# Kernel optimization log

Hardware: AMD Instinct MI355X
Metric: run time of the kernel (lower is better)

Reference implementation:

```python
import jax, jax.numpy as jnp
import numpy as np
from jax import lax

TOP_K = 4
N_GROUP = 4
TOPK_GROUP = 2
ROUTED_SCALING = 2.5
NORM_TOPK = True


def relu2(v):
    r = jax.nn.relu(v)
    return r * r


def setup_inputs() -> dict:
    key = jax.random.key(0)
    ks = jax.random.split(key, 7)
    B, S, H, E, I, IS = 2, 2048, 1024, 16, 512, 2048
    x = jax.random.normal(ks[0], (B, S, H), dtype=jnp.float32)
    router_w = jax.random.normal(ks[1], (E, H), dtype=jnp.float32) * 0.02
    bias = jnp.zeros((E,), dtype=jnp.float32)
    w_up = jax.random.normal(ks[2], (E, I, H), dtype=jnp.float32) * 0.02
    w_down = jax.random.normal(ks[3], (E, H, I), dtype=jnp.float32) * 0.02
    ws_up = jax.random.normal(ks[4], (IS, H), dtype=jnp.float32) * 0.02
    ws_down = jax.random.normal(ks[5], (H, IS), dtype=jnp.float32) * 0.02
    return {"x": x, "router_w": router_w, "bias": bias, "w_up": w_up,
            "w_down": w_down, "ws_up": ws_up, "ws_down": ws_down,
            "attn_metadata": 0}


def _route(xf, router_w, bias):
    # xf: [T, H] float32
    T = xf.shape[0]
    E = router_w.shape[0]
    logits = xf @ router_w.T                      # [T, E]
    scores = jax.nn.sigmoid(logits)
    sfc = scores + bias[None, :]                  # scores_for_choice
    # group scores: sum of top-2 within each group
    g = sfc.reshape(T, N_GROUP, E // N_GROUP)
    group_scores = lax.top_k(g, 2)[0].sum(-1)     # [T, G]
    _, gidx = lax.top_k(group_scores, TOPK_GROUP)
    gmask = jax.nn.one_hot(gidx, N_GROUP, dtype=sfc.dtype).sum(1)  # [T, G]
    smask = jnp.repeat(gmask, E // N_GROUP, axis=1)                # [T, E]
    masked = jnp.where(smask > 0, sfc, 0.0)
    _, tidx = lax.top_k(masked, TOP_K)            # [T, K]
    tw = jnp.take_along_axis(scores, tidx, axis=1)
    if NORM_TOPK:
        tw = tw / (tw.sum(-1, keepdims=True) + 1e-20)
    tw = tw * ROUTED_SCALING
    return tidx, tw


def reference(x, router_w, bias, w_up, w_down, ws_up, ws_down, attn_metadata):
    B, S, H = x.shape
    E = w_up.shape[0]
    xf = x.reshape(-1, H).astype(jnp.float32)     # [T, H]
    tidx, tw = _route(xf, router_w, bias)
    # combine weights per (token, expert): scatter-add topk weights
    T = xf.shape[0]
    comb = jnp.zeros((T, E), dtype=tw.dtype).at[jnp.arange(T)[:, None], tidx].add(tw)
    # routed experts (dense grouped form; zero combine weight == not routed)
    up = jnp.einsum('th,eih->tei', xf, w_up)      # [T, E, I]
    h = relu2(up) * comb[:, :, None]
    routed = jnp.einsum('tei,ehi->th', h, w_down) # [T, H]
    routed = routed.reshape(B, S, H).astype(x.dtype)
    # shared expert on residual
    shared = relu2(jnp.einsum('bsh,ih->bsi', x, ws_up))
    shared = jnp.einsum('bsi,hi->bsh', shared, ws_down)
    return routed + shared
```

## Files before the change

kernel.cpp:

```cpp
#include <hip/hip_runtime.h>
#include <stdint.h>

#define T_TOK 4096
#define H_DIM 1024
#define E_NUM 16
#define I_DIM 512
#define IS_DIM 2048
#define TOPK 4
#define NGRP 4
#define GSZ 4
#define MAXMT 32
#define NCHUNK 64

#define W0 524288
#define W1 1048576
#define W2 3145728
#define W3 5242880

typedef unsigned short u16;
typedef __attribute__((ext_vector_type(8))) short short8;
typedef __attribute__((ext_vector_type(4))) float f32x4;

__device__ __forceinline__ void gload16(const void* g, void* l) {
  __builtin_amdgcn_global_load_lds(
      (const __attribute__((address_space(1))) void*)g,
      (__attribute__((address_space(3))) void*)l, 16, 0, 0);
}

__device__ __forceinline__ u16 f2bf(float f) {
  union { float f; uint32_t u; } v; v.f = f;
  uint32_t u = v.u;
  uint32_t r = (u + 0x7fffu + ((u >> 16) & 1u)) >> 16;
  return (u16)r;
}

__device__ __forceinline__ float bf2f(u16 h) {
  union { uint32_t u; float f; } v; v.u = ((uint32_t)h) << 16;
  return v.f;
}

__global__ __launch_bounds__(256) void cvt_w_kernel(
    const float* __restrict__ wsu, const float* __restrict__ wsd,
    const float* __restrict__ wu, const float* __restrict__ wd,
    u16* __restrict__ wsub, u16* __restrict__ wsdb,
    u16* __restrict__ wub, u16* __restrict__ wdb) {
  int i = blockIdx.x * 256 + threadIdx.x;
  const float4* src; ushort4* dst; int base;
  if (i < W0)      { src = (const float4*)wsu; dst = (ushort4*)wsub; base = 0;  }
  else if (i < W1) { src = (const float4*)wsd; dst = (ushort4*)wsdb; base = W0; }
  else if (i < W2) { src = (const float4*)wu;  dst = (ushort4*)wub;  base = W1; }
  else             { src = (const float4*)wd;  dst = (ushort4*)wdb;  base = W2; }
  float4 v = src[i - base];
  ushort4 o;
  o.x = f2bf(v.x); o.y = f2bf(v.y); o.z = f2bf(v.z); o.w = f2bf(v.w);
  dst[i - base] = o;
}

__global__ __launch_bounds__(256) void route_kernel(
    const float* __restrict__ x, const float* __restrict__ rw,
    const float* __restrict__ bias, int* __restrict__ tidx_out,
    float* __restrict__ tw_out, u16* __restrict__ x_bf) {
  const int wave = threadIdx.x >> 6;
  const int lane = threadIdx.x & 63;
  const int t = blockIdx.x * 4 + wave;

  const float4* xr = reinterpret_cast<const float4*>(x + (size_t)t * H_DIM);
  const float4* rw4 = reinterpret_cast<const float4*>(rw);
  ushort4* xbw = reinterpret_cast<ushort4*>(x_bf + (size_t)t * H_DIM);
  float4 xv[4];
#pragma unroll
  for (int j = 0; j < 4; ++j) xv[j] = xr[lane + j * 64];
#pragma unroll
  for (int j = 0; j < 4; ++j) {
    ushort4 o;
    o.x = f2bf(xv[j].x); o.y = f2bf(xv[j].y);
    o.z = f2bf(xv[j].z); o.w = f2bf(xv[j].w);
    xbw[lane + j * 64] = o;
  }

  double acc[E_NUM];
#pragma unroll
  for (int e = 0; e < E_NUM; ++e) {
    double a = 0.0;
#pragma unroll
    for (int j = 0; j < 4; ++j) {
      float4 w = rw4[e * 256 + lane + j * 64];
      a += (double)xv[j].x * (double)w.x;
      a += (double)xv[j].y * (double)w.y;
      a += (double)xv[j].z * (double)w.z;
      a += (double)xv[j].w * (double)w.w;
    }
    acc[e] = a;
  }
#pragma unroll
  for (int e = 0; e < E_NUM; ++e) {
#pragma unroll
    for (int off = 32; off; off >>= 1) acc[e] += __shfl_xor(acc[e], off);
  }
  if (lane == 0) {
    float scores[E_NUM], sfc[E_NUM];
#pragma unroll
    for (int e = 0; e < E_NUM; ++e) {
      scores[e] = 1.0f / (1.0f + expf((float)(-acc[e])));
      sfc[e] = scores[e] + bias[e];
    }
    float gs[NGRP];
#pragma unroll
    for (int g = 0; g < NGRP; ++g) {
      float m1 = -1e30f, m2 = -1e30f;
#pragma unroll
      for (int j = 0; j < GSZ; ++j) {
        float v = sfc[g * GSZ + j];
        if (v > m1) { m2 = m1; m1 = v; } else if (v > m2) { m2 = v; }
      }
      gs[g] = m1 + m2;
    }
    int g1 = 0;
    for (int g = 1; g < NGRP; ++g) if (gs[g] > gs[g1]) g1 = g;
    int g2 = -1;
    for (int g = 0; g < NGRP; ++g) {
      if (g == g1) continue;
      if (g2 < 0 || gs[g] > gs[g2]) g2 = g;
    }
    float masked[E_NUM];
#pragma unroll
    for (int e = 0; e < E_NUM; ++e) {
      int g = e / GSZ;
      masked[e] = (g == g1 || g == g2) ? sfc[e] : 0.0f;
    }
    int tidx[TOPK]; float tw[TOPK];
#pragma unroll
    for (int k = 0; k < TOPK; ++k) {
      int best = 0; float bv = masked[0];
      for (int e = 1; e < E_NUM; ++e)
        if (masked[e] > bv) { bv = masked[e]; best = e; }
      tidx[k] = best; tw[k] = scores[best]; masked[best] = -1e30f;
    }
    float s = tw[0] + tw[1] + tw[2] + tw[3] + 1e-20f;
#pragma unroll
    for (int k = 0; k < TOPK; ++k) {
      tidx_out[t * TOPK + k] = tidx[k];
      tw_out[t * TOPK + k] = tw[k] / s * 2.5f;
    }
  }
}

__global__ __launch_bounds__(256) void hist_kernel(const int* __restrict__ tidx,
                                                   int* __restrict__ partial) {
  const int c = blockIdx.x;
  const int tid = threadIdx.x;
  const int lane = tid & 63;
  const int w = tid >> 6;
  __shared__ int h[4][E_NUM];
  const int e = tidx[c * 256 + tid];
#pragma unroll
  for (int ee = 0; ee < E_NUM; ++ee) {
    unsigned long long b = __ballot(e == ee);
    if (lane == 0) h[w][ee] = __popcll(b);
  }
  __syncthreads();
  if (tid < E_NUM)
    partial[c * E_NUM + tid] = h[0][tid] + h[1][tid] + h[2][tid] + h[3][tid];
}

__global__ __launch_bounds__(256) void prefix2_kernel(
    const int* __restrict__ partial, int* __restrict__ chunk_base,
    int* __restrict__ counts, int* __restrict__ offsets) {
  __shared__ int tot[E_NUM];
  __shared__ int offs[E_NUM];
  const int tid = threadIdx.x;
  if (tid < E_NUM) {
    int run = 0;
    for (int c = 0; c < NCHUNK; ++c) {
      chunk_base[c * E_NUM + tid] = run;
      run += partial[c * E_NUM + tid];
    }
    tot[tid] = run;
    counts[tid] = run;
  }
  __syncthreads();
  if (tid == 0) {
    int s = 0;
    for (int e = 0; e < E_NUM; ++e) { offs[e] = s; offsets[e] = s; s += tot[e]; }
    offsets[E_NUM] = s;
  }
  __syncthreads();
  for (int i = tid; i < NCHUNK * E_NUM; i += 256)
    chunk_base[i] += offs[i & 15];
}

__global__ __launch_bounds__(256) void scatter2_kernel(
    const int* __restrict__ tidx, const float* __restrict__ tw,
    const int* __restrict__ chunk_base,
    int* __restrict__ tok_g, float* __restrict__ w_g, int* __restrict__ pos_map) {
  const int c = blockIdx.x;
  const int tid = threadIdx.x;
  const int lane = tid & 63;
  const int w = tid >> 6;
  __shared__ int h[4][E_NUM];
  const int i = c * 256 + tid;
  const int e = tidx[i];
  int pre = 0;
#pragma unroll
  for (int ee = 0; ee < E_NUM; ++ee) {
    unsigned long long b = __ballot(e == ee);
    if (lane == 0) h[w][ee] = __popcll(b);
    if (ee == e) pre = __popcll(b & ((1ull << lane) - 1ull));
  }
  __syncthreads();
  int rank = pre;
  for (int ww = 0; ww < w; ++ww) rank += h[ww][e];
  const int pos = chunk_base[c * E_NUM + e] + rank;
  tok_g[pos] = i >> 2;
  w_g[pos] = tw[i];
  pos_map[i] = pos;
}

#define NB_UP 5120
__global__ __launch_bounds__(256, 3) void gemm_up(
    const u16* __restrict__ x_bf, const u16* __restrict__ wsup_bf,
    const u16* __restrict__ wup_bf, u16* __restrict__ hs, u16* __restrict__ hp,
    const int* __restrict__ counts, const int* __restrict__ offsets,
    const int* __restrict__ tok_g, const float* __restrict__ w_g) {
  __shared__ __align__(16) u16 As[2][128 * 64];
  __shared__ __align__(16) u16 Bs[2][64 * 64];

  const int cpx = gridDim.x >> 3;
  const int wg = (blockIdx.x & 7) * cpx + (blockIdx.x >> 3);
  const int q = wg / 5;
  const int r5 = wg - q * 5;
  const bool shared = (r5 == 0);

  int mt, nt, cnt, obase = 0;
  const u16* B;
  if (shared) {
    mt = q >> 5;
    nt = q & 31;
    cnt = T_TOK;
    B = wsup_bf;
  } else {
    int rid = q * 4 + (r5 - 1);
    int e = rid >> 8;
    int r = rid & 255;
    mt = r >> 3;
    nt = r & 7;
    cnt = counts[e];
    if (mt * 128 >= cnt) return;
    obase = offsets[e];
    B = wup_bf + (size_t)e * (I_DIM * H_DIM);
  }
  const int K = H_DIM;

  const int tid = threadIdx.x;
  const int srow = tid >> 3;
  const int slot = tid & 7;
  const u16* gA[4];
#pragma unroll
  for (int p = 0; p < 4; ++p) {
    int rloc = p * 32 + srow;
    int ks = ((slot ^ (rloc & 7)) << 3);
    int am = mt * 128 + rloc;
    int row;
    if (shared) row = am;
    else row = tok_g[obase + ((am < cnt) ? am : 0)];
    gA[p] = x_bf + (size_t)row * H_DIM + ks;
  }
  const u16* gB[2];
#pragma unroll
  for (int p = 0; p < 2; ++p) {
    int rloc = p * 32 + srow;
    int ks = ((slot ^ (rloc & 7)) << 3);
    gB[p] = B + (size_t)(nt * 64 + rloc) * K + ks;
  }

  const int wave = tid >> 6;
  const int lane = tid & 63;
  const int wr = wave >> 1;
  const int wc = wave & 1;
  const int frow = lane & 15;
  const int l4 = lane >> 4;

  int a_off[4][2], b_off[2][2];
#pragma unroll
  for (int m = 0; m < 4; ++m) {
    int row = wr * 64 + m * 16 + frow;
#pragma unroll
    for (int kk = 0; kk < 2; ++kk)
      a_off[m][kk] = (row << 6) + ((((kk << 2) + l4) ^ (row & 7)) << 3);
  }
#pragma unroll
  for (int n = 0; n < 2; ++n) {
    int row = wc * 32 + n * 16 + frow;
#pragma unroll
    for (int kk = 0; kk < 2; ++kk)
      b_off[n][kk] = (row << 6) + ((((kk << 2) + l4) ^ (row & 7)) << 3);
  }

  f32x4 acc[4][2];
#pragma unroll
  for (int m = 0; m < 4; ++m)
#pragma unroll
    for (int n = 0; n < 2; ++n) acc[m][n] = (f32x4)0.0f;

  const int dst = tid << 3;
  auto stage = [&](int k0, int c) {
#pragma unroll
    for (int p = 0; p < 4; ++p)
      gload16(gA[p] + k0, &As[c][(p << 11) + dst]);
#pragma unroll
    for (int p = 0; p < 2; ++p)
      gload16(gB[p] + k0, &Bs[c][(p << 11) + dst]);
  };

  const int KT = K >> 6;
  stage(0, 0);
  int cur = 0;
  for (int kt = 0; kt < KT; ++kt) {
    __syncthreads();
    if (kt + 1 < KT) stage((kt + 1) << 6, cur ^ 1);
#pragma unroll
    for (int kk = 0; kk < 2; ++kk) {
      short8 a[4], b[2];
#pragma unroll
      for (int m = 0; m < 4; ++m)
        a[m] = *reinterpret_cast<const short8*>(&As[cur][a_off[m][kk]]);
#pragma unroll
      for (int n = 0; n < 2; ++n)
        b[n] = *reinterpret_cast<const short8*>(&Bs[cur][b_off[n][kk]]);
      __builtin_amdgcn_s_setprio(1);
#pragma unroll
      for (int m = 0; m < 4; ++m)
#pragma unroll
        for (int n = 0; n < 2; ++n)
          acc[m][n] = __builtin_amdgcn_mfma_f32_16x16x32_bf16(a[m], b[n], acc[m][n], 0, 0, 0);
      __builtin_amdgcn_s_setprio(0);
    }
    cur ^= 1;
  }

  const int rbase = l4 << 2;
  const int cbase = frow;
#pragma unroll
  for (int m = 0; m < 4; ++m) {
#pragma unroll
    for (int r = 0; r < 4; ++r) {
      int lr = wr * 64 + (m << 4) + rbase + r;
      int grow = mt * 128 + lr;
      if (!shared && grow >= cnt) continue;
      float wv = shared ? 1.0f : w_g[obase + grow];
#pragma unroll
      for (int n = 0; n < 2; ++n) {
        int gc = nt * 64 + wc * 32 + (n << 4) + cbase;
        float v = acc[m][n][r];
        float tpos = fmaxf(v, 0.0f);
        float o = tpos * tpos * wv;
        if (shared) hs[(size_t)grow * IS_DIM + gc] = f2bf(o);
        else hp[(size_t)(obase + grow) * I_DIM + gc] = f2bf(o);
      }
    }
  }
}

template <int EPI>
__global__ __launch_bounds__(256, 3) void gemm_bt(
    const u16* __restrict__ Abase, const u16* __restrict__ Bbase,
    float* __restrict__ Cf, u16* __restrict__ Cb,
    int M, int N, int K,
    const int* __restrict__ counts, const int* __restrict__ offsets,
    const int* __restrict__ tok_g, const float* __restrict__ w_g,
    const int* __restrict__ pos_map, const u16* __restrict__ Rd) {
  __shared__ __align__(16) u16 As[2][128 * 64];
  __shared__ __align__(16) u16 Bs[2][64 * 64];

  const int cpx = gridDim.x >> 3;
  const int wg = (blockIdx.x & 7) * cpx + (blockIdx.x >> 3);

  const int NT = N >> 6;
  int mt, nt, cnt = M, obase = 0;
  const u16* A = Abase;
  const u16* B = Bbase;

  if constexpr (EPI == 1) {
    mt = wg / NT;
    nt = wg - mt * NT;
  } else {
    const int per_e = MAXMT * NT;
    int e = wg / per_e;
    int r = wg - e * per_e;
    mt = r / NT;
    nt = r - mt * NT;
    cnt = counts[e];
    if (mt * 128 >= cnt) return;
    obase = offsets[e];
    A = Abase + (size_t)obase * I_DIM;
    B = Bbase + (size_t)e * (H_DIM * I_DIM);
  }

  const int tid = threadIdx.x;
  const int srow = tid >> 3;
  const int slot = tid & 7;
  const u16* gA[4];
#pragma unroll
  for (int p = 0; p < 4; ++p) {
    int rloc = p * 32 + srow;
    int ks = ((slot ^ (rloc & 7)) << 3);
    int am = mt * 128 + rloc;
    if constexpr (EPI == 3) {
      gA[p] = A + (size_t)((am < cnt) ? am : 0) * K + ks;
    } else {
      gA[p] = A + (size_t)am * K + ks;
    }
  }
  const u16* gB[2];
#pragma unroll
  for (int p = 0; p < 2; ++p) {
    int rloc = p * 32 + srow;
    int ks = ((slot ^ (rloc & 7)) << 3);
    gB[p] = B + (size_t)(nt * 64 + rloc) * K + ks;
  }

  const int wave = tid >> 6;
  const int lane = tid & 63;
  const int wr = wave >> 1;
  const int wc = wave & 1;
  const int frow = lane & 15;
  const int l4 = lane >> 4;

  int a_off[4][2], b_off[2][2];
#pragma unroll
  for (int m = 0; m < 4; ++m) {
    int row = wr * 64 + m * 16 + frow;
#pragma unroll
    for (int kk = 0; kk < 2; ++kk)
      a_off[m][kk] = (row << 6) + ((((kk << 2) + l4) ^ (row & 7)) << 3);
  }
#pragma unroll
  for (int n = 0; n < 2; ++n) {
    int row = wc * 32 + n * 16 + frow;
#pragma unroll
    for (int kk = 0; kk < 2; ++kk)
      b_off[n][kk] = (row << 6) + ((((kk << 2) + l4) ^ (row & 7)) << 3);
  }

  f32x4 acc[4][2];
#pragma unroll
  for (int m = 0; m < 4; ++m)
#pragma unroll
    for (int n = 0; n < 2; ++n) acc[m][n] = (f32x4)0.0f;

  const int dst = tid << 3;
  auto stage = [&](int k0, int c) {
#pragma unroll
    for (int p = 0; p < 4; ++p)
      gload16(gA[p] + k0, &As[c][(p << 11) + dst]);
#pragma unroll
    for (int p = 0; p < 2; ++p)
      gload16(gB[p] + k0, &Bs[c][(p << 11) + dst]);
  };

  const int KT = K >> 6;
  stage(0, 0);
  int cur = 0;
  for (int kt = 0; kt < KT; ++kt) {
    __syncthreads();
    if (kt + 1 < KT) stage((kt + 1) << 6, cur ^ 1);
#pragma unroll
    for (int kk = 0; kk < 2; ++kk) {
      short8 a[4], b[2];
#pragma unroll
      for (int m = 0; m < 4; ++m)
        a[m] = *reinterpret_cast<const short8*>(&As[cur][a_off[m][kk]]);
#pragma unroll
      for (int n = 0; n < 2; ++n)
        b[n] = *reinterpret_cast<const short8*>(&Bs[cur][b_off[n][kk]]);
      __builtin_amdgcn_s_setprio(1);
#pragma unroll
      for (int m = 0; m < 4; ++m)
#pragma unroll
        for (int n = 0; n < 2; ++n)
          acc[m][n] = __builtin_amdgcn_mfma_f32_16x16x32_bf16(a[m], b[n], acc[m][n], 0, 0, 0);
      __builtin_amdgcn_s_setprio(0);
    }
    cur ^= 1;
  }

  const int rbase = l4 << 2;
  const int cbase = frow;
#pragma unroll
  for (int m = 0; m < 4; ++m) {
#pragma unroll
    for (int r = 0; r < 4; ++r) {
      int lr = wr * 64 + (m << 4) + rbase + r;
      int grow = mt * 128 + lr;
      if (EPI == 3 && grow >= cnt) continue;
      const int* pm = nullptr;
      if constexpr (EPI == 1) pm = pos_map + grow * TOPK;
#pragma unroll
      for (int n = 0; n < 2; ++n) {
        int gc = nt * 64 + wc * 32 + (n << 4) + cbase;
        float v = acc[m][n][r];
        if constexpr (EPI == 1) {
          v += bf2f(Rd[(size_t)pm[0] * H_DIM + gc]);
          v += bf2f(Rd[(size_t)pm[1] * H_DIM + gc]);
          v += bf2f(Rd[(size_t)pm[2] * H_DIM + gc]);
          v += bf2f(Rd[(size_t)pm[3] * H_DIM + gc]);
          Cf[(size_t)grow * N + gc] = v;
        } else {
          Cb[(size_t)(obase + grow) * N + gc] = f2bf(v);
        }
      }
    }
  }
}

extern "C" void kernel_launch(void* const* d_in, const int* in_sizes, int n_in,
                              void* d_out, int out_size, void* d_ws, size_t ws_size,
                              hipStream_t stream) {
  const float* x = (const float*)d_in[0];
  const float* rw = (const float*)d_in[1];
  const float* bias = (const float*)d_in[2];
  const float* w_up = (const float*)d_in[3];
  const float* w_down = (const float*)d_in[4];
  const float* ws_up = (const float*)d_in[5];
  const float* ws_down = (const float*)d_in[6];
  float* out = (float*)d_out;

  uint8_t* wsb = (uint8_t*)d_ws;
  size_t off = 0;
  auto alloc = [&](size_t bytes) {
    void* p = wsb + off;
    off += (bytes + 255) & ~(size_t)255;
    return p;
  };
  u16* x_bf = (u16*)alloc((size_t)T_TOK * H_DIM * 2);
  u16* wsup_bf = (u16*)alloc((size_t)IS_DIM * H_DIM * 2);
  u16* wsdn_bf = (u16*)alloc((size_t)H_DIM * IS_DIM * 2);
  u16* wup_bf = (u16*)alloc((size_t)E_NUM * I_DIM * H_DIM * 2);
  u16* wdn_bf = (u16*)alloc((size_t)E_NUM * H_DIM * I_DIM * 2);
  u16* hs = (u16*)alloc((size_t)T_TOK * IS_DIM * 2);
  u16* hp = (u16*)alloc((size_t)(T_TOK * TOPK + 128) * I_DIM * 2);
  u16* hp_down = (u16*)alloc((size_t)(T_TOK * TOPK + 128) * H_DIM * 2);
  int* counts = (int*)alloc(64);
  int* offsets = (int*)alloc(128);
  int* tok_g = (int*)alloc((size_t)(T_TOK * TOPK) * 4);
  float* w_g = (float*)alloc((size_t)(T_TOK * TOPK) * 4);
  int* pos_map = (int*)alloc((size_t)(T_TOK * TOPK) * 4);
  int* tidx_buf = (int*)alloc((size_t)T_TOK * TOPK * 4);
  float* tw_buf = (float*)alloc((size_t)T_TOK * TOPK * 4);
  int* partial = (int*)alloc((size_t)NCHUNK * E_NUM * 4);
  int* chunk_base = (int*)alloc((size_t)NCHUNK * E_NUM * 4);

  route_kernel<<<T_TOK / 4, 256, 0, stream>>>(x, rw, bias, tidx_buf, tw_buf, x_bf);
  hist_kernel<<<NCHUNK, 256, 0, stream>>>(tidx_buf, partial);
  prefix2_kernel<<<1, 256, 0, stream>>>(partial, chunk_base, counts, offsets);
  scatter2_kernel<<<NCHUNK, 256, 0, stream>>>(tidx_buf, tw_buf, chunk_base,
                                              tok_g, w_g, pos_map);
  cvt_w_kernel<<<W3 / 256, 256, 0, stream>>>(
      ws_up, ws_down, w_up, w_down, wsup_bf, wsdn_bf, wup_bf, wdn_bf);

  gemm_up<<<NB_UP, 256, 0, stream>>>(
      x_bf, wsup_bf, wup_bf, hs, hp, counts, offsets, tok_g, w_g);
  gemm_bt<3><<<E_NUM * MAXMT * (H_DIM / 64), 256, 0, stream>>>(
      hp, wdn_bf, nullptr, hp_down, T_TOK, H_DIM, I_DIM,
      counts, offsets, tok_g, w_g, nullptr, nullptr);
  gemm_bt<1><<<(T_TOK / 128) * (H_DIM / 64), 256, 0, stream>>>(
      hs, wsdn_bf, out, nullptr, T_TOK, H_DIM, IS_DIM,
      nullptr, nullptr, nullptr, nullptr, pos_map, hp_down);
}
```

Baseline: 194.2 us.

## Switch GEMM mainloops to 3-stage BK=32 pipeline with fine-grained vmcnt waits

Both the up-projection and generic GEMM kernels move from a double-buffered BK=64 tile to a triple-buffered BK=32 tile with a matching swizzle. Loads are issued two stages ahead, and each step waits with an explicit s_waitcnt vmcnt instead of a full __syncthreads drain. Shared memory per block drops from 48KB to 36KB, and launch bounds rise to 4 blocks per CU for better latency hiding. The trade-off is twice as many barriers and loop iterations, each with fewer MFMAs, and reliance on a hand-counted vmcnt being correct.

```diff
diff --git a/kernel.cpp b/kernel.cpp
--- a/kernel.cpp
+++ b/kernel.cpp
@@ -217,13 +217,13 @@
 }
 
 #define NB_UP 5120
-__global__ __launch_bounds__(256, 3) void gemm_up(
+__global__ __launch_bounds__(256, 4) void gemm_up(
     const u16* __restrict__ x_bf, const u16* __restrict__ wsup_bf,
     const u16* __restrict__ wup_bf, u16* __restrict__ hs, u16* __restrict__ hp,
     const int* __restrict__ counts, const int* __restrict__ offsets,
     const int* __restrict__ tok_g, const float* __restrict__ w_g) {
-  __shared__ __align__(16) u16 As[2][128 * 64];
-  __shared__ __align__(16) u16 Bs[2][64 * 64];
+  __shared__ __align__(16) u16 As[3][128 * 32];
+  __shared__ __align__(16) u16 Bs[3][64 * 32];
 
   const int cpx = gridDim.x >> 3;
   const int wg = (blockIdx.x & 7) * cpx + (blockIdx.x >> 3);
@@ -252,25 +252,23 @@
   const int K = H_DIM;
 
   const int tid = threadIdx.x;
-  const int srow = tid >> 3;
-  const int slot = tid & 7;
-  const u16* gA[4];
-#pragma unroll
-  for (int p = 0; p < 4; ++p) {
-    int rloc = p * 32 + srow;
-    int ks = ((slot ^ (rloc & 7)) << 3);
+  const int srow = tid >> 2;
+  const int sphys = tid & 3;
+  const u16* gA[2];
+#pragma unroll
+  for (int p = 0; p < 2; ++p) {
+    int rloc = p * 64 + srow;
+    int ks = ((sphys ^ ((rloc >> 1) & 3)) << 3);
     int am = mt * 128 + rloc;
     int row;
     if (shared) row = am;
     else row = tok_g[obase + ((am < cnt) ? am : 0)];
     gA[p] = x_bf + (size_t)row * H_DIM + ks;
   }
-  const u16* gB[2];
-#pragma unroll
-  for (int p = 0; p < 2; ++p) {
-    int rloc = p * 32 + srow;
-    int ks = ((slot ^ (rloc & 7)) << 3);
-    gB[p] = B + (size_t)(nt * 64 + rloc) * K + ks;
+  const u16* gB;
+  {
+    int ks = ((sphys ^ ((srow >> 1) & 3)) << 3);
+    gB = B + (size_t)(nt * 64 + srow) * K + ks;
   }
 
   const int wave = tid >> 6;
@@ -280,20 +278,16 @@
   const int frow = lane & 15;
   const int l4 = lane >> 4;
 
-  int a_off[4][2], b_off[2][2];
+  int a_off[4], b_off[2];
 #pragma unroll
   for (int m = 0; m < 4; ++m) {
     int row = wr * 64 + m * 16 + frow;
-#pragma unroll
-    for (int kk = 0; kk < 2; ++kk)
-      a_off[m][kk] = (row << 6) + ((((kk << 2) + l4) ^ (row & 7)) << 3);
+    a_off[m] = (row << 5) + ((l4 ^ ((row >> 1) & 3)) << 3);
   }
 #pragma unroll
   for (int n = 0; n < 2; ++n) {
     int row = wc * 32 + n * 16 + frow;
-#pragma unroll
-    for (int kk = 0; kk < 2; ++kk)
-      b_off[n][kk] = (row << 6) + ((((kk << 2) + l4) ^ (row & 7)) << 3);
+    b_off[n] = (row << 5) + ((l4 ^ ((row >> 1) & 3)) << 3);
   }
 
   f32x4 acc[4][2];
@@ -305,37 +299,40 @@
   const int dst = tid << 3;
   auto stage = [&](int k0, int c) {
 #pragma unroll
-    for (int p = 0; p < 4; ++p)
+    for (int p = 0; p < 2; ++p)
       gload16(gA[p] + k0, &As[c][(p << 11) + dst]);
-#pragma unroll
-    for (int p = 0; p < 2; ++p)
-      gload16(gB[p] + k0, &Bs[c][(p << 11) + dst]);
+    gload16(gB + k0, &Bs[c][dst]);
   };
 
-  const int KT = K >> 6;
+  const int KT = K >> 5;
   stage(0, 0);
-  int cur = 0;
+  stage(32, 1);
+  int cb = 0, sb = 2;
   for (int kt = 0; kt < KT; ++kt) {
-    __syncthreads();
-    if (kt + 1 < KT) stage((kt + 1) << 6, cur ^ 1);
-#pragma unroll
-    for (int kk = 0; kk < 2; ++kk) {
-      short8 a[4], b[2];
-#pragma unroll
-      for (int m = 0; m < 4; ++m)
-        a[m] = *reinterpret_cast<const short8*>(&As[cur][a_off[m][kk]]);
+    if (kt < KT - 1) {
+      asm volatile("s_waitcnt vmcnt(3)" ::: "memory");
+    } else {
+      asm volatile("s_waitcnt vmcnt(0)" ::: "memory");
+    }
+    __builtin_amdgcn_s_barrier();
+    __builtin_amdgcn_sched_barrier(0);
+    if (kt + 2 < KT) stage((kt + 2) << 5, sb);
+    short8 a[4], b[2];
+#pragma unroll
+    for (int m = 0; m < 4; ++m)
+      a[m] = *reinterpret_cast<const short8*>(&As[cb][a_off[m]]);
+#pragma unroll
+    for (int n = 0; n < 2; ++n)
+      b[n] = *reinterpret_cast<const short8*>(&Bs[cb][b_off[n]]);
+    __builtin_amdgcn_s_setprio(1);
+#pragma unroll
+    for (int m = 0; m < 4; ++m)
 #pragma unroll
       for (int n = 0; n < 2; ++n)
-        b[n] = *reinterpret_cast<const short8*>(&Bs[cur][b_off[n][kk]]);
-      __builtin_amdgcn_s_setprio(1);
-#pragma unroll
-      for (int m = 0; m < 4; ++m)
-#pragma unroll
-        for (int n = 0; n < 2; ++n)
-          acc[m][n] = __builtin_amdgcn_mfma_f32_16x16x32_bf16(a[m], b[n], acc[m][n], 0, 0, 0);
-      __builtin_amdgcn_s_setprio(0);
-    }
-    cur ^= 1;
+        acc[m][n] = __builtin_amdgcn_mfma_f32_16x16x32_bf16(a[m], b[n], acc[m][n], 0, 0, 0);
+    __builtin_amdgcn_s_setprio(0);
+    cb = (cb == 2) ? 0 : cb + 1;
+    sb = (sb == 2) ? 0 : sb + 1;
   }
 
   const int rbase = l4 << 2;
@@ -362,15 +359,15 @@
 }
 
 template <int EPI>
-__global__ __launch_bounds__(256, 3) void gemm_bt(
+__global__ __launch_bounds__(256, 4) void gemm_bt(
     const u16* __restrict__ Abase, const u16* __restrict__ Bbase,
     float* __restrict__ Cf, u16* __restrict__ Cb,
     int M, int N, int K,
     const int* __restrict__ counts, const int* __restrict__ offsets,
     const int* __restrict__ tok_g, const float* __restrict__ w_g,
     const int* __restrict__ pos_map, const u16* __restrict__ Rd) {
-  __shared__ __align__(16) u16 As[2][128 * 64];
-  __shared__ __align__(16) u16 Bs[2][64 * 64];
+  __shared__ __align__(16) u16 As[3][128 * 32];
+  __shared__ __align__(16) u16 Bs[3][64 * 32];
 
   const int cpx = gridDim.x >> 3;
   const int wg = (blockIdx.x & 7) * cpx + (blockIdx.x >> 3);
@@ -397,13 +394,13 @@
   }
 
   const int tid = threadIdx.x;
-  const int srow = tid >> 3;
-  const int slot = tid & 7;
-  const u16* gA[4];
-#pragma unroll
-  for (int p = 0; p < 4; ++p) {
-    int rloc = p * 32 + srow;
-    int ks = ((slot ^ (rloc & 7)) << 3);
+  const int srow = tid >> 2;
+  const int sphys = tid & 3;
+  const u16* gA[2];
+#pragma unroll
+  for (int p = 0; p < 2; ++p) {
+    int rloc = p * 64 + srow;
+    int ks = ((sphys ^ ((rloc >> 1) & 3)) << 3);
     int am = mt * 128 + rloc;
     if constexpr (EPI == 3) {
       gA[p] = A + (size_t)((am < cnt) ? am : 0) * K + ks;
@@ -411,12 +408,10 @@
       gA[p] = A + (size_t)am * K + ks;
     }
   }
-  const u16* gB[2];
-#pragma unroll
-  for (int p = 0; p < 2; ++p) {
-    int rloc = p * 32 + srow;
-    int ks = ((slot ^ (rloc & 7)) << 3);
-    gB[p] = B + (size_t)(nt * 64 + rloc) * K + ks;
+  const u16* gB;
+  {
+    int ks = ((sphys ^ ((srow >> 1) & 3)) << 3);
+    gB = B + (size_t)(nt * 64 + srow) * K + ks;
   }
 
   const int wave = tid >> 6;
@@ -426,20 +421,16 @@
   const int frow = lane & 15;
   const int l4 = lane >> 4;
 
-  int a_off[4][2], b_off[2][2];
+  int a_off[4], b_off[2];
 #pragma unroll
   for (int m = 0; m < 4; ++m) {
     int row = wr * 64 + m * 16 + frow;
-#pragma unroll
-    for (int kk = 0; kk < 2; ++kk)
-      a_off[m][kk] = (row << 6) + ((((kk << 2) + l4) ^ (row & 7)) << 3);
+    a_off[m] = (row << 5) + ((l4 ^ ((row >> 1) & 3)) << 3);
   }
 #pragma unroll
   for (int n = 0; n < 2; ++n) {
     int row = wc * 32 + n * 16 + frow;
-#pragma unroll
-    for (int kk = 0; kk < 2; ++kk)
-      b_off[n][kk] = (row << 6) + ((((kk << 2) + l4) ^ (row & 7)) << 3);
+    b_off[n] = (row << 5) + ((l4 ^ ((row >> 1) & 3)) << 3);
   }
 
   f32x4 acc[4][2];
@@ -451,37 +442,40 @@
   const int dst = tid << 3;
   auto stage = [&](int k0, int c) {
 #pragma unroll
-    for (int p = 0; p < 4; ++p)
+    for (int p = 0; p < 2; ++p)
       gload16(gA[p] + k0, &As[c][(p << 11) + dst]);
-#pragma unroll
-    for (int p = 0; p < 2; ++p)
-      gload16(gB[p] + k0, &Bs[c][(p << 11) + dst]);
+    gload16(gB + k0, &Bs[c][dst]);
   };
 
-  const int KT = K >> 6;
+  const int KT = K >> 5;
   stage(0, 0);
-  int cur = 0;
+  stage(32, 1);
+  int cb = 0, sb = 2;
   for (int kt = 0; kt < KT; ++kt) {
-    __syncthreads();
-    if (kt + 1 < KT) stage((kt + 1) << 6, cur ^ 1);
-#pragma unroll
-    for (int kk = 0; kk < 2; ++kk) {
-      short8 a[4], b[2];
-#pragma unroll
-      for (int m = 0; m < 4; ++m)
-        a[m] = *reinterpret_cast<const short8*>(&As[cur][a_off[m][kk]]);
+    if (kt < KT - 1) {
+      asm volatile("s_waitcnt vmcnt(3)" ::: "memory");
+    } else {
+      asm volatile("s_waitcnt vmcnt(0)" ::: "memory");
+    }
+    __builtin_amdgcn_s_barrier();
+    __builtin_amdgcn_sched_barrier(0);
+    if (kt + 2 < KT) stage((kt + 2) << 5, sb);
+    short8 a[4], b[2];
+#pragma unroll
+    for (int m = 0; m < 4; ++m)
+      a[m] = *reinterpret_cast<const short8*>(&As[cb][a_off[m]]);
+#pragma unroll
+    for (int n = 0; n < 2; ++n)
+      b[n] = *reinterpret_cast<const short8*>(&Bs[cb][b_off[n]]);
+    __builtin_amdgcn_s_setprio(1);
+#pragma unroll
+    for (int m = 0; m < 4; ++m)
 #pragma unroll
       for (int n = 0; n < 2; ++n)
-        b[n] = *reinterpret_cast<const short8*>(&Bs[cur][b_off[n][kk]]);
-      __builtin_amdgcn_s_setprio(1);
-#pragma unroll
-      for (int m = 0; m < 4; ++m)
-#pragma unroll
-        for (int n = 0; n < 2; ++n)
-          acc[m][n] = __builtin_amdgcn_mfma_f32_16x16x32_bf16(a[m], b[n], acc[m][n], 0, 0, 0);
-      __builtin_amdgcn_s_setprio(0);
-    }
-    cur ^= 1;
+        acc[m][n] = __builtin_amdgcn_mfma_f32_16x16x32_bf16(a[m], b[n], acc[m][n], 0, 0, 0);
+    __builtin_amdgcn_s_setprio(0);
+    cb = (cb == 2) ? 0 : cb + 1;
+    sb = (sb == 2) ? 0 : sb + 1;
   }
 
   const int rbase = l4 << 2;
```

Measured after the change: 221.4 us. 14.0% more time.

## Overlap down-weight bf16 conversion with up-projection GEMM blocks

Applied to the files above, without the earlier changes.

The single weight-conversion kernel is split. Only the up-projection weights are converted before gemm_up, and conversion of the down-projection weights moves into extra blocks of gemm_up, interleaved one in three. This lets the memory-bound conversion run alongside the compute-bound GEMM tiles, so it no longer sits serially on the critical path. The cost is a larger grid, where conversion blocks take occupancy slots and share the same launch-bounds register budget. Tile index remapping also changes the block order.

```diff
diff --git a/kernel.cpp b/kernel.cpp
--- a/kernel.cpp
+++ b/kernel.cpp
@@ -12,10 +12,13 @@
 #define MAXMT 32
 #define NCHUNK 64
 
-#define W0 524288
-#define W1 1048576
-#define W2 3145728
-#define W3 5242880
+#define WSU_F4 524288
+#define WU_F4 2097152
+#define CVTUP_NB ((WSU_F4 + WU_F4) / 256)
+#define WSD_F4 524288
+#define WD_F4 2097152
+#define NB_UP 5120
+#define NB_UP2 7680
 
 typedef unsigned short u16;
 typedef __attribute__((ext_vector_type(8))) short short8;
@@ -39,21 +42,17 @@
   return v.f;
 }
 
-__global__ __launch_bounds__(256) void cvt_w_kernel(
-    const float* __restrict__ wsu, const float* __restrict__ wsd,
-    const float* __restrict__ wu, const float* __restrict__ wd,
-    u16* __restrict__ wsub, u16* __restrict__ wsdb,
-    u16* __restrict__ wub, u16* __restrict__ wdb) {
+__global__ __launch_bounds__(256) void cvt_up_kernel(
+    const float* __restrict__ wsu, const float* __restrict__ wu,
+    u16* __restrict__ wsub, u16* __restrict__ wub) {
   int i = blockIdx.x * 256 + threadIdx.x;
-  const float4* src; ushort4* dst; int base;
-  if (i < W0)      { src = (const float4*)wsu; dst = (ushort4*)wsub; base = 0;  }
-  else if (i < W1) { src = (const float4*)wsd; dst = (ushort4*)wsdb; base = W0; }
-  else if (i < W2) { src = (const float4*)wu;  dst = (ushort4*)wub;  base = W1; }
-  else             { src = (const float4*)wd;  dst = (ushort4*)wdb;  base = W2; }
-  float4 v = src[i - base];
+  const float4* src; ushort4* dst;
+  if (i < WSU_F4) { src = (const float4*)wsu; dst = (ushort4*)wsub; }
+  else { src = (const float4*)wu; dst = (ushort4*)wub; i -= WSU_F4; }
+  float4 v = src[i];
   ushort4 o;
   o.x = f2bf(v.x); o.y = f2bf(v.y); o.z = f2bf(v.z); o.w = f2bf(v.w);
-  dst[i - base] = o;
+  dst[i] = o;
 }
 
 __global__ __launch_bounds__(256) void route_kernel(
@@ -216,19 +215,44 @@
   pos_map[i] = pos;
 }
 
-#define NB_UP 5120
 __global__ __launch_bounds__(256, 3) void gemm_up(
     const u16* __restrict__ x_bf, const u16* __restrict__ wsup_bf,
     const u16* __restrict__ wup_bf, u16* __restrict__ hs, u16* __restrict__ hp,
     const int* __restrict__ counts, const int* __restrict__ offsets,
-    const int* __restrict__ tok_g, const float* __restrict__ w_g) {
+    const int* __restrict__ tok_g, const float* __restrict__ w_g,
+    const float* __restrict__ wsd, const float* __restrict__ wd,
+    u16* __restrict__ wsdb, u16* __restrict__ wdb) {
   __shared__ __align__(16) u16 As[2][128 * 64];
   __shared__ __align__(16) u16 Bs[2][64 * 64];
 
   const int cpx = gridDim.x >> 3;
   const int wg = (blockIdx.x & 7) * cpx + (blockIdx.x >> 3);
-  const int q = wg / 5;
-  const int r5 = wg - q * 5;
+  const int q3 = wg / 3;
+  const int r3 = wg - q3 * 3;
+
+  if (r3 == 2) {
+    int base = q3 * 1024 + threadIdx.x;
+#pragma unroll
+    for (int j = 0; j < 4; ++j) {
+      int i = base + j * 256;
+      float4 v; ushort4 o;
+      if (i < WSD_F4) {
+        v = reinterpret_cast<const float4*>(wsd)[i];
+        o.x = f2bf(v.x); o.y = f2bf(v.y); o.z = f2bf(v.z); o.w = f2bf(v.w);
+        reinterpret_cast<ushort4*>(wsdb)[i] = o;
+      } else {
+        int k = i - WSD_F4;
+        v = reinterpret_cast<const float4*>(wd)[k];
+        o.x = f2bf(v.x); o.y = f2bf(v.y); o.z = f2bf(v.z); o.w = f2bf(v.w);
+        reinterpret_cast<ushort4*>(wdb)[k] = o;
+      }
+    }
+    return;
+  }
+
+  const int g = q3 * 2 + r3;
+  const int q = g / 5;
+  const int r5 = g - q * 5;
   const bool shared = (r5 == 0);
 
   int mt, nt, cnt, obase = 0;
@@ -555,11 +579,11 @@
   prefix2_kernel<<<1, 256, 0, stream>>>(partial, chunk_base, counts, offsets);
   scatter2_kernel<<<NCHUNK, 256, 0, stream>>>(tidx_buf, tw_buf, chunk_base,
                                               tok_g, w_g, pos_map);
-  cvt_w_kernel<<<W3 / 256, 256, 0, stream>>>(
-      ws_up, ws_down, w_up, w_down, wsup_bf, wsdn_bf, wup_bf, wdn_bf);
-
-  gemm_up<<<NB_UP, 256, 0, stream>>>(
-      x_bf, wsup_bf, wup_bf, hs, hp, counts, offsets, tok_g, w_g);
+  cvt_up_kernel<<<CVTUP_NB, 256, 0, stream>>>(ws_up, w_up, wsup_bf, wup_bf);
+
+  gemm_up<<<NB_UP2, 256, 0, stream>>>(
+      x_bf, wsup_bf, wup_bf, hs, hp, counts, offsets, tok_g, w_g,
+      ws_down, w_down, wsdn_bf, wdn_bf);
   gemm_bt<3><<<E_NUM * MAXMT * (H_DIM / 64), 256, 0, stream>>>(
       hp, wdn_bf, nullptr, hp_down, T_TOK, H_DIM, I_DIM,
       counts, offsets, tok_g, w_g, nullptr, nullptr);
```

New measurement: 196.3 us. About the same (+1.1%).
